# Performance work log

Hardware: AMD Instinct MI355X
Metric: run time of the kernel (lower is better)

The kernel has to match this reference:

```python
import jax, jax.numpy as jnp
import numpy as np

BEAMS, TEMP, DEPTH, K = 8, 0.4, 3, 3   # beams, router temperature, max_depth, n_experts
EPS, NEG = 1e-5, -1e9

def _conv(x, w, b):
    y = jax.lax.conv_general_dilated(x, w, (1, 1), 'VALID',
                                     dimension_numbers=('NCHW', 'OIHW', 'NCHW'))
    return y + b[None, :, None, None]

def _bn(x, g, b, m, v):
    inv = g * jax.lax.rsqrt(v + EPS)
    return x * inv[None, :, None, None] + (b - m * inv)[None, :, None, None]

def _pool(x):  # AvgPool2d(2)
    return jax.lax.reduce_window(x, 0.0, jax.lax.add, (1, 1, 2, 2), (1, 1, 2, 2), 'VALID') * 0.25

def _fwd(x, conv1_w, conv1_b, bn1_g, bn1_b, bn1_m, bn1_v,
         conv2_w, conv2_b, bn2_g, bn2_b, bn2_m, bn2_v,
         conv3_w, conv3_b, bn3_g, bn3_b, bn3_m, bn3_v,
         Wxh, Whh, bh, Who, bo, emb, Wexp, bexp, Wout, bout):
    B = x.shape[0]
    h = _pool(jax.nn.relu(_bn(_conv(x, conv1_w, conv1_b), bn1_g, bn1_b, bn1_m, bn1_v)))
    h = _pool(jax.nn.relu(_bn(_conv(h, conv2_w, conv2_b), bn2_g, bn2_b, bn2_m, bn2_v)))
    h = _pool(jax.nn.relu(_bn(_conv(h, conv3_w, conv3_b), bn3_g, bn3_b, bn3_m, bn3_v)))
    feat = h.reshape(B, -1)                                  # (B,128)
    # --- beam search over length-3 op sequences with RNN router ---
    hr = jnp.broadcast_to(feat[:, None, :], (B, BEAMS, 128))  # router hidden, (B,beams,128)
    scores = jnp.full((B, BEAMS), NEG, dtype=x.dtype).at[:, 0].set(0.0)
    ops_seq = []
    for _ in range(DEPTH):
        logits = jnp.einsum('bkd,do->bko', hr, Who) + bo      # (B,beams,3)
        logp = jax.nn.log_softmax(logits / TEMP, axis=-1)
        total = (scores[..., None] + logp).reshape(B, BEAMS * K)
        scores, idx = jax.lax.top_k(total, BEAMS)             # (B,beams)
        beam_idx, op = idx // K, idx % K
        hr = jnp.take_along_axis(hr, beam_idx[..., None], axis=1)
        hr = jnp.tanh(hr @ Whh + emb[op] @ Wxh + bh)
        ops_seq = [jnp.take_along_axis(o, beam_idx, axis=1) for o in ops_seq]
        ops_seq.append(op)
    # --- top-1 routed expert chain (grouped gather-GEMM instead of per-sample loop) ---
    hs = jnp.broadcast_to(feat[:, None, :], (B, BEAMS, 128)).reshape(B * BEAMS, 128)
    for op in ops_seq:
        o = op.reshape(B * BEAMS)
        hs = jax.nn.relu(jnp.einsum('nd,ndk->nk', hs, Wexp[o]) + bexp[o])
    return jax.nn.log_softmax(hs @ Wout + bout, axis=1)      # (B*beams,10)

def setup_inputs() -> dict:
    key = jax.random.key(0)
    ks = jax.random.split(key, 20)
    n = lambda i, shape, s: jax.random.normal(ks[i], shape, jnp.float32) * s
    d = {
        'x': jax.random.normal(ks[0], (512, 1, 32, 32), jnp.float32),
        'conv1_w': n(1, (32, 1, 3, 3), 0.2),  'conv1_b': n(2, (32,), 0.02),
        'bn1_g': jnp.ones((32,), jnp.float32), 'bn1_b': jnp.zeros((32,), jnp.float32),
        'bn1_m': jnp.zeros((32,), jnp.float32), 'bn1_v': jnp.ones((32,), jnp.float32),
        'conv2_w': n(3, (32, 32, 3, 3), 0.06), 'conv2_b': n(4, (32,), 0.02),
        'bn2_g': jnp.ones((32,), jnp.float32), 'bn2_b': jnp.zeros((32,), jnp.float32),
        'bn2_m': jnp.zeros((32,), jnp.float32), 'bn2_v': jnp.ones((32,), jnp.float32),
        'conv3_w': n(5, (32, 32, 3, 3), 0.06), 'conv3_b': n(6, (32,), 0.02),
        'bn3_g': jnp.ones((32,), jnp.float32), 'bn3_b': jnp.zeros((32,), jnp.float32),
        'bn3_m': jnp.zeros((32,), jnp.float32), 'bn3_v': jnp.ones((32,), jnp.float32),
        'Wxh': n(7, (128, 128), 0.09), 'Whh': n(8, (128, 128), 0.09), 'bh': n(9, (128,), 0.02),
        'Who': n(10, (128, 3), 0.09), 'bo': n(11, (3,), 0.02), 'emb': n(12, (3, 128), 0.5),
        'Wexp': n(13, (3, 128, 128), 0.09), 'bexp': n(14, (3, 128), 0.02),
        'Wout': n(15, (128, 10), 0.09), 'bout': n(16, (10,), 0.02),
    }
    return d

def reference(x, conv1_w, conv1_b, bn1_g, bn1_b, bn1_m, bn1_v,
              conv2_w, conv2_b, bn2_g, bn2_b, bn2_m, bn2_v,
              conv3_w, conv3_b, bn3_g, bn3_b, bn3_m, bn3_v,
              Wxh, Whh, bh, Who, bo, emb, Wexp, bexp, Wout, bout):
    return _fwd(x, conv1_w, conv1_b, bn1_g, bn1_b, bn1_m, bn1_v,
                conv2_w, conv2_b, bn2_g, bn2_b, bn2_m, bn2_v,
                conv3_w, conv3_b, bn3_g, bn3_b, bn3_m, bn3_v,
                Wxh, Whh, bh, Who, bo, emb, Wexp, bexp, Wout, bout)
```

## Files before the change

kernel.cpp:

```cpp
#include <hip/hip_runtime.h>
#include <math.h>

__global__ __launch_bounds__(512) void conv1_k(
    const float* __restrict__ x, const float* __restrict__ w,
    const float* __restrict__ cb, const float* __restrict__ bg,
    const float* __restrict__ bb, const float* __restrict__ bm,
    const float* __restrict__ bv, float* __restrict__ h1)
{
    __shared__ float img[32 * 33];
    __shared__ float ws_[288];
    __shared__ float scale[32], bias2[32];
    const int b = blockIdx.x, tid = threadIdx.x;
    for (int i = tid; i < 1024; i += 512) {
        const int y = i >> 5, xx = i & 31;
        img[y * 33 + xx] = x[b * 1024 + i];
    }
    if (tid < 288) ws_[tid] = w[tid];
    if (tid < 32) {
        float inv = bg[tid] / sqrtf(bv[tid] + 1e-5f);
        scale[tid] = inv;
        bias2[tid] = (cb[tid] - bm[tid]) * inv + bb[tid];
    }
    __syncthreads();

    const int co = tid >> 4, py = tid & 15;
    if (py < 15) {
        float acc0[30], acc1[30];
        #pragma unroll
        for (int i = 0; i < 30; ++i) { acc0[i] = 0.f; acc1[i] = 0.f; }
        const float* w9 = &ws_[co * 9];
        #pragma unroll
        for (int ir = 0; ir < 4; ++ir) {
            const int y = 2 * py + ir;
            float wk0 = 0.f, wk1 = 0.f, wk2 = 0.f, wl0 = 0.f, wl1 = 0.f, wl2 = 0.f;
            if (ir <= 2) { wk0 = w9[ir * 3 + 0]; wk1 = w9[ir * 3 + 1]; wk2 = w9[ir * 3 + 2]; }
            if (ir >= 1) { wl0 = w9[(ir - 1) * 3 + 0]; wl1 = w9[(ir - 1) * 3 + 1]; wl2 = w9[(ir - 1) * 3 + 2]; }
            #pragma unroll
            for (int xx = 0; xx < 32; ++xx) {
                const float rv = img[y * 33 + xx];
                if (ir <= 2) {
                    if (xx <= 29) acc0[xx] += rv * wk0;
                    if (xx >= 1 && xx <= 30) acc0[xx - 1] += rv * wk1;
                    if (xx >= 2) acc0[xx - 2] += rv * wk2;
                }
                if (ir >= 1) {
                    if (xx <= 29) acc1[xx] += rv * wl0;
                    if (xx >= 1 && xx <= 30) acc1[xx - 1] += rv * wl1;
                    if (xx >= 2) acc1[xx - 2] += rv * wl2;
                }
            }
        }
        const float sc = scale[co], bs = bias2[co];
        #pragma unroll
        for (int px = 0; px < 15; ++px) {
            const float v = fmaxf(acc0[2 * px] * sc + bs, 0.f)
                          + fmaxf(acc0[2 * px + 1] * sc + bs, 0.f)
                          + fmaxf(acc1[2 * px] * sc + bs, 0.f)
                          + fmaxf(acc1[2 * px + 1] * sc + bs, 0.f);
            h1[b * 7200 + co * 225 + py * 15 + px] = v * 0.25f;
        }
    }
}

__global__ __launch_bounds__(384) void conv2_k(
    const float* __restrict__ h1, const float* __restrict__ w,
    const float* __restrict__ cb, const float* __restrict__ bg,
    const float* __restrict__ bb, const float* __restrict__ bm,
    const float* __restrict__ bv, float* __restrict__ h2)
{
    __shared__ float in_s[32 * 210];
    __shared__ float w_s[9216];
    __shared__ float scale[32], bias2[32];
    const int b = blockIdx.x, tid = threadIdx.x;
    for (int i = tid; i < 6720; i += 384) {
        const int ci = i / 210, rem = i % 210;
        in_s[i] = h1[b * 7200 + ci * 225 + rem];
    }
    for (int i = tid; i < 9216; i += 384) {
        const int co = i & 31, k = i >> 5;
        w_s[i] = w[co * 288 + k];
    }
    if (tid < 32) {
        float inv = bg[tid] / sqrtf(bv[tid] + 1e-5f);
        scale[tid] = inv;
        bias2[tid] = (cb[tid] - bm[tid]) * inv + bb[tid];
    }
    __syncthreads();

    const int co = tid & 31, g = tid >> 5;
    const int py = g >> 1, xh = g & 1;
    const int gx0 = xh * 6;
    float acc0[6], acc1[6];
    #pragma unroll
    for (int i = 0; i < 6; ++i) { acc0[i] = 0.f; acc1[i] = 0.f; }

    for (int ci = 0; ci < 32; ++ci) {
        float w9[9];
        #pragma unroll
        for (int kk = 0; kk < 9; ++kk) w9[kk] = w_s[(ci * 9 + kk) * 32 + co];
        const float* ip = &in_s[ci * 210];
        #pragma unroll
        for (int ir = 0; ir < 4; ++ir) {
            const int y = 2 * py + ir;
            const float* rowp = &ip[y * 15 + gx0];
            #pragma unroll
            for (int xx = 0; xx < 8; ++xx) {
                const float rv = rowp[xx];
                if (ir <= 2) {
                    if (xx <= 5) acc0[xx] += rv * w9[ir * 3 + 0];
                    if (xx >= 1 && xx <= 6) acc0[xx - 1] += rv * w9[ir * 3 + 1];
                    if (xx >= 2) acc0[xx - 2] += rv * w9[ir * 3 + 2];
                }
                if (ir >= 1) {
                    if (xx <= 5) acc1[xx] += rv * w9[(ir - 1) * 3 + 0];
                    if (xx >= 1 && xx <= 6) acc1[xx - 1] += rv * w9[(ir - 1) * 3 + 1];
                    if (xx >= 2) acc1[xx - 2] += rv * w9[(ir - 1) * 3 + 2];
                }
            }
        }
    }
    const float sc = scale[co], bs = bias2[co];
    #pragma unroll
    for (int pxl = 0; pxl < 3; ++pxl) {
        const float v = fmaxf(acc0[2 * pxl] * sc + bs, 0.f)
                      + fmaxf(acc0[2 * pxl + 1] * sc + bs, 0.f)
                      + fmaxf(acc1[2 * pxl] * sc + bs, 0.f)
                      + fmaxf(acc1[2 * pxl + 1] * sc + bs, 0.f);
        h2[b * 1152 + co * 36 + py * 6 + xh * 3 + pxl] = v * 0.25f;
    }
}

__global__ __launch_bounds__(256) void conv3_k(
    const float* __restrict__ h2, const float* __restrict__ w,
    const float* __restrict__ cb, const float* __restrict__ bg,
    const float* __restrict__ bb, const float* __restrict__ bm,
    const float* __restrict__ bv, float* __restrict__ feat)
{
    __shared__ float in_s[1152];
    __shared__ float w_s[9216];
    __shared__ float psum[2][4][4][33];
    __shared__ float scale[32], bias2[32];
    const int b = blockIdx.x, tid = threadIdx.x;
    for (int i = tid; i < 1152; i += 256) in_s[i] = h2[b * 1152 + i];
    for (int i = tid; i < 9216; i += 256) {
        const int co = i & 31, k = i >> 5;
        w_s[i] = w[co * 288 + k];
    }
    if (tid < 32) {
        float inv = bg[tid] / sqrtf(bv[tid] + 1e-5f);
        scale[tid] = inv;
        bias2[tid] = (cb[tid] - bm[tid]) * inv + bb[tid];
    }
    __syncthreads();

    const int co = tid & 31, g = tid >> 5;
    const int pos = g & 3, h = g >> 2;
    const int y0 = (pos >> 1) * 2, x0 = (pos & 1) * 2;
    float s00 = 0.f, s01 = 0.f, s10 = 0.f, s11 = 0.f;
    for (int ci = h * 16; ci < h * 16 + 16; ++ci) {
        float w9[9];
        #pragma unroll
        for (int kk = 0; kk < 9; ++kk) w9[kk] = w_s[(ci * 9 + kk) * 32 + co];
        const float* ip = &in_s[ci * 36 + y0 * 6 + x0];
        float p[4][4];
        #pragma unroll
        for (int i = 0; i < 4; ++i)
            #pragma unroll
            for (int j = 0; j < 4; ++j)
                p[i][j] = ip[i * 6 + j];
        #pragma unroll
        for (int ky = 0; ky < 3; ++ky)
            #pragma unroll
            for (int kx = 0; kx < 3; ++kx) {
                const float wv = w9[ky * 3 + kx];
                s00 += p[ky][kx] * wv;
                s01 += p[ky][kx + 1] * wv;
                s10 += p[ky + 1][kx] * wv;
                s11 += p[ky + 1][kx + 1] * wv;
            }
    }
    psum[h][pos][0][co] = s00;
    psum[h][pos][1][co] = s01;
    psum[h][pos][2][co] = s10;
    psum[h][pos][3][co] = s11;
    __syncthreads();
    if (h == 0) {
        const float sc = scale[co], bs = bias2[co];
        float v = 0.f;
        #pragma unroll
        for (int k = 0; k < 4; ++k) {
            const float sk = psum[0][pos][k][co] + psum[1][pos][k][co];
            v += fmaxf(sk * sc + bs, 0.f);
        }
        feat[b * 128 + co * 4 + pos] = v * 0.25f;
    }
}

__global__ __launch_bounds__(384) void e2_k(
    const float* __restrict__ emb, const float* __restrict__ Wxh,
    const float* __restrict__ bh, float* __restrict__ E2)
{
    const int t = threadIdx.x;
    const int o = t >> 7, j = t & 127;
    float a = bh[j];
    float a2 = 0.f;
    #pragma unroll 4
    for (int d = 0; d < 64; ++d) {
        a  += emb[o * 128 + d] * Wxh[d * 128 + j];
        a2 += emb[o * 128 + d + 64] * Wxh[(d + 64) * 128 + j];
    }
    E2[t] = a + a2;
}

__global__ __launch_bounds__(512, 4) void router_k(
    const float* __restrict__ feat, const float* __restrict__ Whh,
    const float* __restrict__ Who, const float* __restrict__ bo,
    const float* __restrict__ E2, const float* __restrict__ Wexp,
    const float* __restrict__ bexp, const float* __restrict__ Wout,
    const float* __restrict__ bout, float* __restrict__ out)
{
    const int b = blockIdx.x, tid = threadIdx.x;
    const int j = tid & 127, q = tid >> 7;
    __shared__ float hbuf[2][8][128];
    __shared__ float E2s[3][128];
    __shared__ float bexps[3][128];
    __shared__ float psum[4][8][128];
    __shared__ float total[24], scores[8];
    __shared__ int bi[8], opsel[8], oph[3][8], oph2[3][8];

    const float fv = feat[b * 128 + j];
    hbuf[0][2 * q][j] = fv;
    hbuf[0][2 * q + 1][j] = fv;
    for (int i = tid; i < 384; i += 512) {
        (&E2s[0][0])[i] = E2[i];
        (&bexps[0][0])[i] = bexp[i];
    }
    if (tid < 8) scores[tid] = (tid == 0) ? 0.f : -1.0e9f;
    __syncthreads();

    int cur = 0;
    for (int t = 0; t < 3; ++t) {
        {
            const int grp = tid >> 5, l = tid & 31;
            if (grp < 8) {
                float p0 = 0.f, p1 = 0.f, p2 = 0.f;
                #pragma unroll
                for (int dd = 0; dd < 4; ++dd) {
                    const int d = l + 32 * dd;
                    const float hv = hbuf[cur][grp][d];
                    p0 += hv * Who[d * 3 + 0];
                    p1 += hv * Who[d * 3 + 1];
                    p2 += hv * Who[d * 3 + 2];
                }
                #pragma unroll
                for (int s = 16; s > 0; s >>= 1) {
                    p0 += __shfl_down(p0, s, 32);
                    p1 += __shfl_down(p1, s, 32);
                    p2 += __shfl_down(p2, s, 32);
                }
                if (l == 0) {
                    const float t0 = (p0 + bo[0]) / 0.4f;
                    const float t1 = (p1 + bo[1]) / 0.4f;
                    const float t2 = (p2 + bo[2]) / 0.4f;
                    const float mm = fmaxf(t0, fmaxf(t1, t2));
                    const float lse = mm + logf(expf(t0 - mm) + expf(t1 - mm) + expf(t2 - mm));
                    const float sc = scores[grp];
                    total[grp * 3 + 0] = sc + (t0 - lse);
                    total[grp * 3 + 1] = sc + (t1 - lse);
                    total[grp * 3 + 2] = sc + (t2 - lse);
                }
            }
        }
        __syncthreads();
        if (tid == 0) {
            float tv[24];
            #pragma unroll
            for (int i = 0; i < 24; ++i) tv[i] = total[i];
            unsigned mask = 0;
            for (int r = 0; r < 8; ++r) {
                float best = -INFINITY; int idx = 0;
                #pragma unroll
                for (int i = 0; i < 24; ++i) {
                    if (!(mask & (1u << i)) && tv[i] > best) { best = tv[i]; idx = i; }
                }
                mask |= 1u << idx;
                scores[r] = best;
                bi[r] = idx / 3;
                opsel[r] = idx % 3;
            }
            for (int r = 0; r < 8; ++r) {
                for (int s = 0; s < t; ++s) oph2[s][r] = oph[s][bi[r]];
                oph2[t][r] = opsel[r];
            }
            for (int r = 0; r < 8; ++r)
                for (int s = 0; s <= t; ++s) oph[s][r] = oph2[s][r];
        }
        __syncthreads();
        {
            const float* h0 = &hbuf[cur][bi[0]][0];
            const float* h1 = &hbuf[cur][bi[1]][0];
            const float* h2 = &hbuf[cur][bi[2]][0];
            const float* h3 = &hbuf[cur][bi[3]][0];
            const float* h4 = &hbuf[cur][bi[4]][0];
            const float* h5 = &hbuf[cur][bi[5]][0];
            const float* h6 = &hbuf[cur][bi[6]][0];
            const float* h7 = &hbuf[cur][bi[7]][0];
            float a0 = 0.f, a1 = 0.f, a2 = 0.f, a3 = 0.f, a4 = 0.f, a5 = 0.f, a6 = 0.f, a7 = 0.f;
            const int dbase = q * 32;
            const float* wp = &Whh[dbase * 128 + j];
            #pragma unroll 4
            for (int dd = 0; dd < 32; ++dd) {
                const int d = dbase + dd;
                const float wv = wp[dd * 128];
                a0 += h0[d] * wv; a1 += h1[d] * wv; a2 += h2[d] * wv; a3 += h3[d] * wv;
                a4 += h4[d] * wv; a5 += h5[d] * wv; a6 += h6[d] * wv; a7 += h7[d] * wv;
            }
            psum[q][0][j] = a0; psum[q][1][j] = a1; psum[q][2][j] = a2; psum[q][3][j] = a3;
            psum[q][4][j] = a4; psum[q][5][j] = a5; psum[q][6][j] = a6; psum[q][7][j] = a7;
        }
        __syncthreads();
        {
            const int nxt = cur ^ 1;
            #pragma unroll
            for (int rr = 0; rr < 2; ++rr) {
                const int r = 2 * q + rr;
                const float v = psum[0][r][j] + psum[1][r][j] + psum[2][r][j] + psum[3][r][j]
                              + E2s[opsel[r]][j];
                hbuf[nxt][r][j] = tanhf(v);
            }
        }
        cur ^= 1;
        __syncthreads();
    }

    hbuf[0][2 * q][j] = fv;
    hbuf[0][2 * q + 1][j] = fv;
    __syncthreads();
    int c2 = 0;
    for (int t = 0; t < 3; ++t) {
        const int o0 = oph[t][0], o1 = oph[t][1], o2 = oph[t][2], o3 = oph[t][3];
        const int o4 = oph[t][4], o5 = oph[t][5], o6 = oph[t][6], o7 = oph[t][7];
        {
            const float* h0 = &hbuf[c2][0][0];
            const float* h1 = &hbuf[c2][1][0];
            const float* h2 = &hbuf[c2][2][0];
            const float* h3 = &hbuf[c2][3][0];
            const float* h4 = &hbuf[c2][4][0];
            const float* h5 = &hbuf[c2][5][0];
            const float* h6 = &hbuf[c2][6][0];
            const float* h7 = &hbuf[c2][7][0];
            float a0 = 0.f, a1 = 0.f, a2 = 0.f, a3 = 0.f, a4 = 0.f, a5 = 0.f, a6 = 0.f, a7 = 0.f;
            const int dbase = q * 32;
            const float* wp = &Wexp[dbase * 128 + j];
            #pragma unroll 4
            for (int dd = 0; dd < 32; ++dd) {
                const int d = dbase + dd;
                const float w0 = wp[dd * 128];
                const float w1 = wp[dd * 128 + 16384];
                const float w2 = wp[dd * 128 + 32768];
                a0 += h0[d] * (o0 == 2 ? w2 : (o0 == 1 ? w1 : w0));
                a1 += h1[d] * (o1 == 2 ? w2 : (o1 == 1 ? w1 : w0));
                a2 += h2[d] * (o2 == 2 ? w2 : (o2 == 1 ? w1 : w0));
                a3 += h3[d] * (o3 == 2 ? w2 : (o3 == 1 ? w1 : w0));
                a4 += h4[d] * (o4 == 2 ? w2 : (o4 == 1 ? w1 : w0));
                a5 += h5[d] * (o5 == 2 ? w2 : (o5 == 1 ? w1 : w0));
                a6 += h6[d] * (o6 == 2 ? w2 : (o6 == 1 ? w1 : w0));
                a7 += h7[d] * (o7 == 2 ? w2 : (o7 == 1 ? w1 : w0));
            }
            psum[q][0][j] = a0; psum[q][1][j] = a1; psum[q][2][j] = a2; psum[q][3][j] = a3;
            psum[q][4][j] = a4; psum[q][5][j] = a5; psum[q][6][j] = a6; psum[q][7][j] = a7;
        }
        __syncthreads();
        {
            const int nxt = c2 ^ 1;
            #pragma unroll
            for (int rr = 0; rr < 2; ++rr) {
                const int r = 2 * q + rr;
                const float v = psum[0][r][j] + psum[1][r][j] + psum[2][r][j] + psum[3][r][j]
                              + bexps[oph[t][r]][j];
                hbuf[nxt][r][j] = fmaxf(v, 0.f);
            }
        }
        c2 ^= 1;
        __syncthreads();
    }

    {
        const int grp = tid >> 5, l = tid & 31;
        if (grp < 8) {
            float acc = 0.f;
            if (l < 10) {
                acc = bout[l];
                float acc2 = 0.f;
                const float* hrow = &hbuf[c2][grp][0];
                #pragma unroll 4
                for (int d = 0; d < 64; ++d) {
                    acc  += hrow[d] * Wout[d * 10 + l];
                    acc2 += hrow[d + 64] * Wout[(d + 64) * 10 + l];
                }
                acc += acc2;
            }
            float mm = (l < 10) ? acc : -INFINITY;
            #pragma unroll
            for (int s = 16; s > 0; s >>= 1) mm = fmaxf(mm, __shfl_xor(mm, s, 32));
            float ex = (l < 10) ? expf(acc - mm) : 0.f;
            float sum = ex;
            #pragma unroll
            for (int s = 16; s > 0; s >>= 1) sum += __shfl_xor(sum, s, 32);
            const float lse = mm + logf(sum);
            if (l < 10) out[(b * 8 + grp) * 10 + l] = acc - lse;
        }
    }
}

extern "C" void kernel_launch(void* const* d_in, const int* in_sizes, int n_in,
                              void* d_out, int out_size, void* d_ws, size_t ws_size,
                              hipStream_t stream) {
    (void)in_sizes; (void)n_in; (void)out_size; (void)ws_size;
    const float* x    = (const float*)d_in[0];
    const float* c1w  = (const float*)d_in[1];
    const float* c1b  = (const float*)d_in[2];
    const float* g1   = (const float*)d_in[3];
    const float* b1   = (const float*)d_in[4];
    const float* m1   = (const float*)d_in[5];
    const float* v1   = (const float*)d_in[6];
    const float* c2w  = (const float*)d_in[7];
    const float* c2b  = (const float*)d_in[8];
    const float* g2   = (const float*)d_in[9];
    const float* b2   = (const float*)d_in[10];
    const float* m2   = (const float*)d_in[11];
    const float* v2   = (const float*)d_in[12];
    const float* c3w  = (const float*)d_in[13];
    const float* c3b  = (const float*)d_in[14];
    const float* g3   = (const float*)d_in[15];
    const float* b3   = (const float*)d_in[16];
    const float* m3   = (const float*)d_in[17];
    const float* v3   = (const float*)d_in[18];
    const float* Wxh  = (const float*)d_in[19];
    const float* Whh  = (const float*)d_in[20];
    const float* bh   = (const float*)d_in[21];
    const float* Who  = (const float*)d_in[22];
    const float* bo   = (const float*)d_in[23];
    const float* emb  = (const float*)d_in[24];
    const float* Wexp = (const float*)d_in[25];
    const float* bexp = (const float*)d_in[26];
    const float* Wout = (const float*)d_in[27];
    const float* bout = (const float*)d_in[28];

    float* ws   = (float*)d_ws;
    float* h1   = ws;
    float* h2   = h1 + 3686400;
    float* feat = h2 + 589824;
    float* E2   = feat + 65536;

    e2_k<<<1, 384, 0, stream>>>(emb, Wxh, bh, E2);
    conv1_k<<<512, 512, 0, stream>>>(x, c1w, c1b, g1, b1, m1, v1, h1);
    conv2_k<<<512, 384, 0, stream>>>(h1, c2w, c2b, g2, b2, m2, v2, h2);
    conv3_k<<<512, 256, 0, stream>>>(h2, c3w, c3b, g3, b3, m3, v3, feat);
    router_k<<<512, 512, 0, stream>>>(feat, Whh, Who, bo, E2,
                                      Wexp, bexp, Wout, bout, (float*)d_out);
}
```

Baseline: 244.9 us.

## Pre-transpose conv weights once, restructure conv2 tiling, use readlane broadcasts in router

```diff
diff --git a/kernel.cpp b/kernel.cpp
--- a/kernel.cpp
+++ b/kernel.cpp
@@ -1,5 +1,38 @@
 #include <hip/hip_runtime.h>
 #include <math.h>
+
+__device__ __forceinline__ float rdlane(float v, int l) {
+    return __int_as_float(__builtin_amdgcn_readlane(__float_as_int(v), l));
+}
+
+__global__ __launch_bounds__(384) void wprep_k(
+    const float* __restrict__ c2w, const float* __restrict__ c3w,
+    const float* __restrict__ emb, const float* __restrict__ Wxh,
+    const float* __restrict__ bh,
+    float* __restrict__ w2t, float* __restrict__ w3t, float* __restrict__ E2)
+{
+    const int t = threadIdx.x, blk = blockIdx.x;
+    if (blk == 0) {
+        for (int i = t; i < 9216; i += 384) {
+            const int co = i & 31, k = i >> 5;
+            w2t[i] = c2w[co * 288 + k];
+        }
+    } else if (blk == 1) {
+        for (int i = t; i < 9216; i += 384) {
+            const int co = i & 31, k = i >> 5;
+            w3t[i] = c3w[co * 288 + k];
+        }
+    } else {
+        const int o = t >> 7, j = t & 127;
+        float a = bh[j], a2 = 0.f;
+        #pragma unroll 4
+        for (int d = 0; d < 64; ++d) {
+            a  += emb[o * 128 + d] * Wxh[d * 128 + j];
+            a2 += emb[o * 128 + d + 64] * Wxh[(d + 64) * 128 + j];
+        }
+        E2[t] = a + a2;
+    }
+}
 
 __global__ __launch_bounds__(512) void conv1_k(
     const float* __restrict__ x, const float* __restrict__ w,
@@ -62,94 +95,82 @@
     }
 }
 
-__global__ __launch_bounds__(384) void conv2_k(
-    const float* __restrict__ h1, const float* __restrict__ w,
+__global__ __launch_bounds__(192) void conv2_k(
+    const float* __restrict__ h1, const float* __restrict__ w2t,
     const float* __restrict__ cb, const float* __restrict__ bg,
     const float* __restrict__ bb, const float* __restrict__ bm,
     const float* __restrict__ bv, float* __restrict__ h2)
 {
-    __shared__ float in_s[32 * 210];
-    __shared__ float w_s[9216];
-    __shared__ float scale[32], bias2[32];
+    __shared__ float in_s[32 * 14 * 16];
     const int b = blockIdx.x, tid = threadIdx.x;
-    for (int i = tid; i < 6720; i += 384) {
+    for (int i = tid; i < 6720; i += 192) {
         const int ci = i / 210, rem = i % 210;
-        in_s[i] = h1[b * 7200 + ci * 225 + rem];
-    }
-    for (int i = tid; i < 9216; i += 384) {
-        const int co = i & 31, k = i >> 5;
-        w_s[i] = w[co * 288 + k];
-    }
-    if (tid < 32) {
-        float inv = bg[tid] / sqrtf(bv[tid] + 1e-5f);
-        scale[tid] = inv;
-        bias2[tid] = (cb[tid] - bm[tid]) * inv + bb[tid];
-    }
-    __syncthreads();
-
-    const int co = tid & 31, g = tid >> 5;
-    const int py = g >> 1, xh = g & 1;
-    const int gx0 = xh * 6;
-    float acc0[6], acc1[6];
+        const int row = rem / 15, col = rem % 15;
+        in_s[ci * 224 + row * 16 + col] = h1[b * 7200 + ci * 225 + rem];
+    }
+    __syncthreads();
+
+    const int co = tid & 31, py = tid >> 5;
+    float acc0[12], acc1[12];
     #pragma unroll
-    for (int i = 0; i < 6; ++i) { acc0[i] = 0.f; acc1[i] = 0.f; }
+    for (int i = 0; i < 12; ++i) { acc0[i] = 0.f; acc1[i] = 0.f; }
 
     for (int ci = 0; ci < 32; ++ci) {
         float w9[9];
-        #pragma unroll
-        for (int kk = 0; kk < 9; ++kk) w9[kk] = w_s[(ci * 9 + kk) * 32 + co];
-        const float* ip = &in_s[ci * 210];
+        const float* wk = &w2t[(ci * 9) * 32 + co];
+        #pragma unroll
+        for (int kk = 0; kk < 9; ++kk) w9[kk] = wk[kk * 32];
         #pragma unroll
         for (int ir = 0; ir < 4; ++ir) {
-            const int y = 2 * py + ir;
-            const float* rowp = &ip[y * 15 + gx0];
-            #pragma unroll
-            for (int xx = 0; xx < 8; ++xx) {
-                const float rv = rowp[xx];
-                if (ir <= 2) {
-                    if (xx <= 5) acc0[xx] += rv * w9[ir * 3 + 0];
-                    if (xx >= 1 && xx <= 6) acc0[xx - 1] += rv * w9[ir * 3 + 1];
-                    if (xx >= 2) acc0[xx - 2] += rv * w9[ir * 3 + 2];
-                }
-                if (ir >= 1) {
-                    if (xx <= 5) acc1[xx] += rv * w9[(ir - 1) * 3 + 0];
-                    if (xx >= 1 && xx <= 6) acc1[xx - 1] += rv * w9[(ir - 1) * 3 + 1];
-                    if (xx >= 2) acc1[xx - 2] += rv * w9[(ir - 1) * 3 + 2];
-                }
-            }
-        }
-    }
-    const float sc = scale[co], bs = bias2[co];
+            const float* rp = &in_s[ci * 224 + (2 * py + ir) * 16];
+            const float4 q0 = *reinterpret_cast<const float4*>(rp);
+            const float4 q1 = *reinterpret_cast<const float4*>(rp + 4);
+            const float4 q2 = *reinterpret_cast<const float4*>(rp + 8);
+            const float4 q3 = *reinterpret_cast<const float4*>(rp + 12);
+            float p[16];
+            p[0]=q0.x; p[1]=q0.y; p[2]=q0.z; p[3]=q0.w;
+            p[4]=q1.x; p[5]=q1.y; p[6]=q1.z; p[7]=q1.w;
+            p[8]=q2.x; p[9]=q2.y; p[10]=q2.z; p[11]=q2.w;
+            p[12]=q3.x; p[13]=q3.y; p[14]=q3.z; p[15]=q3.w;
+            if (ir <= 2) {
+                const float wa0 = w9[ir * 3], wa1 = w9[ir * 3 + 1], wa2 = w9[ir * 3 + 2];
+                #pragma unroll
+                for (int c = 0; c < 12; ++c)
+                    acc0[c] += p[c] * wa0 + p[c + 1] * wa1 + p[c + 2] * wa2;
+            }
+            if (ir >= 1) {
+                const float wb0 = w9[(ir - 1) * 3], wb1 = w9[(ir - 1) * 3 + 1], wb2 = w9[(ir - 1) * 3 + 2];
+                #pragma unroll
+                for (int c = 0; c < 12; ++c)
+                    acc1[c] += p[c] * wb0 + p[c + 1] * wb1 + p[c + 2] * wb2;
+            }
+        }
+    }
+    const float inv = bg[co] / sqrtf(bv[co] + 1e-5f);
+    const float bs = (cb[co] - bm[co]) * inv + bb[co];
     #pragma unroll
-    for (int pxl = 0; pxl < 3; ++pxl) {
-        const float v = fmaxf(acc0[2 * pxl] * sc + bs, 0.f)
-                      + fmaxf(acc0[2 * pxl + 1] * sc + bs, 0.f)
-                      + fmaxf(acc1[2 * pxl] * sc + bs, 0.f)
-                      + fmaxf(acc1[2 * pxl + 1] * sc + bs, 0.f);
-        h2[b * 1152 + co * 36 + py * 6 + xh * 3 + pxl] = v * 0.25f;
+    for (int px = 0; px < 6; ++px) {
+        const float v = fmaxf(acc0[2 * px] * inv + bs, 0.f)
+                      + fmaxf(acc0[2 * px + 1] * inv + bs, 0.f)
+                      + fmaxf(acc1[2 * px] * inv + bs, 0.f)
+                      + fmaxf(acc1[2 * px + 1] * inv + bs, 0.f);
+        h2[b * 1152 + co * 36 + py * 6 + px] = v * 0.25f;
     }
 }
 
 __global__ __launch_bounds__(256) void conv3_k(
-    const float* __restrict__ h2, const float* __restrict__ w,
+    const float* __restrict__ h2, const float* __restrict__ w3t,
     const float* __restrict__ cb, const float* __restrict__ bg,
     const float* __restrict__ bb, const float* __restrict__ bm,
     const float* __restrict__ bv, float* __restrict__ feat)
 {
-    __shared__ float in_s[1152];
-    __shared__ float w_s[9216];
+    __shared__ float in_s[32 * 48];
     __shared__ float psum[2][4][4][33];
-    __shared__ float scale[32], bias2[32];
     const int b = blockIdx.x, tid = threadIdx.x;
-    for (int i = tid; i < 1152; i += 256) in_s[i] = h2[b * 1152 + i];
-    for (int i = tid; i < 9216; i += 256) {
-        const int co = i & 31, k = i >> 5;
-        w_s[i] = w[co * 288 + k];
-    }
-    if (tid < 32) {
-        float inv = bg[tid] / sqrtf(bv[tid] + 1e-5f);
-        scale[tid] = inv;
-        bias2[tid] = (cb[tid] - bm[tid]) * inv + bb[tid];
+    for (int i = tid; i < 1152; i += 256) {
+        const int ci = i / 36, rem = i % 36;
+        const int row = rem / 6, col = rem % 6;
+        in_s[ci * 48 + row * 8 + col] = h2[b * 1152 + i];
     }
     __syncthreads();
 
@@ -159,15 +180,17 @@
     float s00 = 0.f, s01 = 0.f, s10 = 0.f, s11 = 0.f;
     for (int ci = h * 16; ci < h * 16 + 16; ++ci) {
         float w9[9];
-        #pragma unroll
-        for (int kk = 0; kk < 9; ++kk) w9[kk] = w_s[(ci * 9 + kk) * 32 + co];
-        const float* ip = &in_s[ci * 36 + y0 * 6 + x0];
+        const float* wk = &w3t[(ci * 9) * 32 + co];
+        #pragma unroll
+        for (int kk = 0; kk < 9; ++kk) w9[kk] = wk[kk * 32];
+        const int base = ci * 48 + y0 * 8 + x0;
         float p[4][4];
         #pragma unroll
-        for (int i = 0; i < 4; ++i)
-            #pragma unroll
-            for (int j = 0; j < 4; ++j)
-                p[i][j] = ip[i * 6 + j];
+        for (int i = 0; i < 4; ++i) {
+            const float2 a = *reinterpret_cast<const float2*>(&in_s[base + i * 8]);
+            const float2 c = *reinterpret_cast<const float2*>(&in_s[base + i * 8 + 2]);
+            p[i][0] = a.x; p[i][1] = a.y; p[i][2] = c.x; p[i][3] = c.y;
+        }
         #pragma unroll
         for (int ky = 0; ky < 3; ++ky)
             #pragma unroll
@@ -185,31 +208,16 @@
     psum[h][pos][3][co] = s11;
     __syncthreads();
     if (h == 0) {
-        const float sc = scale[co], bs = bias2[co];
+        const float inv = bg[co] / sqrtf(bv[co] + 1e-5f);
+        const float bs = (cb[co] - bm[co]) * inv + bb[co];
         float v = 0.f;
         #pragma unroll
         for (int k = 0; k < 4; ++k) {
             const float sk = psum[0][pos][k][co] + psum[1][pos][k][co];
-            v += fmaxf(sk * sc + bs, 0.f);
+            v += fmaxf(sk * inv + bs, 0.f);
         }
         feat[b * 128 + co * 4 + pos] = v * 0.25f;
     }
-}
-
-__global__ __launch_bounds__(384) void e2_k(
-    const float* __restrict__ emb, const float* __restrict__ Wxh,
-    const float* __restrict__ bh, float* __restrict__ E2)
-{
-    const int t = threadIdx.x;
-    const int o = t >> 7, j = t & 127;
-    float a = bh[j];
-    float a2 = 0.f;
-    #pragma unroll 4
-    for (int d = 0; d < 64; ++d) {
-        a  += emb[o * 128 + d] * Wxh[d * 128 + j];
-        a2 += emb[o * 128 + d + 64] * Wxh[(d + 64) * 128 + j];
-    }
-    E2[t] = a + a2;
 }
 
 __global__ __launch_bounds__(512, 4) void router_k(
@@ -220,7 +228,7 @@
     const float* __restrict__ bout, float* __restrict__ out)
 {
     const int b = blockIdx.x, tid = threadIdx.x;
-    const int j = tid & 127, q = tid >> 7;
+    const int j = tid & 127, q = tid >> 7, lane31 = tid & 31;
     __shared__ float hbuf[2][8][128];
     __shared__ float E2s[3][128];
     __shared__ float bexps[3][128];
@@ -238,6 +246,7 @@
     if (tid < 8) scores[tid] = (tid == 0) ? 0.f : -1.0e9f;
     __syncthreads();
 
+    const int dbase = q * 32;
     int cur = 0;
     for (int t = 0; t < 3; ++t) {
         {
@@ -297,23 +306,23 @@
         }
         __syncthreads();
         {
-            const float* h0 = &hbuf[cur][bi[0]][0];
-            const float* h1 = &hbuf[cur][bi[1]][0];
-            const float* h2 = &hbuf[cur][bi[2]][0];
-            const float* h3 = &hbuf[cur][bi[3]][0];
-            const float* h4 = &hbuf[cur][bi[4]][0];
-            const float* h5 = &hbuf[cur][bi[5]][0];
-            const float* h6 = &hbuf[cur][bi[6]][0];
-            const float* h7 = &hbuf[cur][bi[7]][0];
+            const float h0r = hbuf[cur][bi[0]][dbase + lane31];
+            const float h1r = hbuf[cur][bi[1]][dbase + lane31];
+            const float h2r = hbuf[cur][bi[2]][dbase + lane31];
+            const float h3r = hbuf[cur][bi[3]][dbase + lane31];
+            const float h4r = hbuf[cur][bi[4]][dbase + lane31];
+            const float h5r = hbuf[cur][bi[5]][dbase + lane31];
+            const float h6r = hbuf[cur][bi[6]][dbase + lane31];
+            const float h7r = hbuf[cur][bi[7]][dbase + lane31];
             float a0 = 0.f, a1 = 0.f, a2 = 0.f, a3 = 0.f, a4 = 0.f, a5 = 0.f, a6 = 0.f, a7 = 0.f;
-            const int dbase = q * 32;
             const float* wp = &Whh[dbase * 128 + j];
-            #pragma unroll 4
+            #pragma unroll
             for (int dd = 0; dd < 32; ++dd) {
-                const int d = dbase + dd;
                 const float wv = wp[dd * 128];
-                a0 += h0[d] * wv; a1 += h1[d] * wv; a2 += h2[d] * wv; a3 += h3[d] * wv;
-                a4 += h4[d] * wv; a5 += h5[d] * wv; a6 += h6[d] * wv; a7 += h7[d] * wv;
+                a0 += rdlane(h0r, dd) * wv; a1 += rdlane(h1r, dd) * wv;
+                a2 += rdlane(h2r, dd) * wv; a3 += rdlane(h3r, dd) * wv;
+                a4 += rdlane(h4r, dd) * wv; a5 += rdlane(h5r, dd) * wv;
+                a6 += rdlane(h6r, dd) * wv; a7 += rdlane(h7r, dd) * wv;
             }
             psum[q][0][j] = a0; psum[q][1][j] = a1; psum[q][2][j] = a2; psum[q][3][j] = a3;
             psum[q][4][j] = a4; psum[q][5][j] = a5; psum[q][6][j] = a6; psum[q][7][j] = a7;
@@ -338,34 +347,34 @@
     __syncthreads();
     int c2 = 0;
     for (int t = 0; t < 3; ++t) {
-        const int o0 = oph[t][0], o1 = oph[t][1], o2 = oph[t][2], o3 = oph[t][3];
-        const int o4 = oph[t][4], o5 = oph[t][5], o6 = oph[t][6], o7 = oph[t][7];
         {
-            const float* h0 = &hbuf[c2][0][0];
-            const float* h1 = &hbuf[c2][1][0];
-            const float* h2 = &hbuf[c2][2][0];
-            const float* h3 = &hbuf[c2][3][0];
-            const float* h4 = &hbuf[c2][4][0];
-            const float* h5 = &hbuf[c2][5][0];
-            const float* h6 = &hbuf[c2][6][0];
-            const float* h7 = &hbuf[c2][7][0];
+            const float h0r = hbuf[c2][0][dbase + lane31];
+            const float h1r = hbuf[c2][1][dbase + lane31];
+            const float h2r = hbuf[c2][2][dbase + lane31];
+            const float h3r = hbuf[c2][3][dbase + lane31];
+            const float h4r = hbuf[c2][4][dbase + lane31];
+            const float h5r = hbuf[c2][5][dbase + lane31];
+            const float h6r = hbuf[c2][6][dbase + lane31];
+            const float h7r = hbuf[c2][7][dbase + lane31];
+            const float* wp0 = &Wexp[oph[t][0] * 16384 + dbase * 128 + j];
+            const float* wp1 = &Wexp[oph[t][1] * 16384 + dbase * 128 + j];
+            const float* wp2 = &Wexp[oph[t][2] * 16384 + dbase * 128 + j];
+            const float* wp3 = &Wexp[oph[t][3] * 16384 + dbase * 128 + j];
+            const float* wp4 = &Wexp[oph[t][4] * 16384 + dbase * 128 + j];
+            const float* wp5 = &Wexp[oph[t][5] * 16384 + dbase * 128 + j];
+            const float* wp6 = &Wexp[oph[t][6] * 16384 + dbase * 128 + j];
+            const float* wp7 = &Wexp[oph[t][7] * 16384 + dbase * 128 + j];
             float a0 = 0.f, a1 = 0.f, a2 = 0.f, a3 = 0.f, a4 = 0.f, a5 = 0.f, a6 = 0.f, a7 = 0.f;
-            const int dbase = q * 32;
-            const float* wp = &Wexp[dbase * 128 + j];
-            #pragma unroll 4
+            #pragma unroll
             for (int dd = 0; dd < 32; ++dd) {
-                const int d = dbase + dd;
-                const float w0 = wp[dd * 128];
-                const float w1 = wp[dd * 128 + 16384];
-                const float w2 = wp[dd * 128 + 32768];
-                a0 += h0[d] * (o0 == 2 ? w2 : (o0 == 1 ? w1 : w0));
-                a1 += h1[d] * (o1 == 2 ? w2 : (o1 == 1 ? w1 : w0));
-                a2 += h2[d] * (o2 == 2 ? w2 : (o2 == 1 ? w1 : w0));
-                a3 += h3[d] * (o3 == 2 ? w2 : (o3 == 1 ? w1 : w0));
-                a4 += h4[d] * (o4 == 2 ? w2 : (o4 == 1 ? w1 : w0));
-                a5 += h5[d] * (o5 == 2 ? w2 : (o5 == 1 ? w1 : w0));
-                a6 += h6[d] * (o6 == 2 ? w2 : (o6 == 1 ? w1 : w0));
-                a7 += h7[d] * (o7 == 2 ? w2 : (o7 == 1 ? w1 : w0));
+                a0 += rdlane(h0r, dd) * wp0[dd * 128];
+                a1 += rdlane(h1r, dd) * wp1[dd * 128];
+                a2 += rdlane(h2r, dd) * wp2[dd * 128];
+                a3 += rdlane(h3r, dd) * wp3[dd * 128];
+                a4 += rdlane(h4r, dd) * wp4[dd * 128];
+                a5 += rdlane(h5r, dd) * wp5[dd * 128];
+                a6 += rdlane(h6r, dd) * wp6[dd * 128];
+                a7 += rdlane(h7r, dd) * wp7[dd * 128];
             }
             psum[q][0][j] = a0; psum[q][1][j] = a1; psum[q][2][j] = a2; psum[q][3][j] = a3;
             psum[q][4][j] = a4; psum[q][5][j] = a5; psum[q][6][j] = a6; psum[q][7][j] = a7;
@@ -452,11 +461,13 @@
     float* h2   = h1 + 3686400;
     float* feat = h2 + 589824;
     float* E2   = feat + 65536;
-
-    e2_k<<<1, 384, 0, stream>>>(emb, Wxh, bh, E2);
+    float* w2t  = E2 + 384;
+    float* w3t  = w2t + 9216;
+
+    wprep_k<<<3, 384, 0, stream>>>(c2w, c3w, emb, Wxh, bh, w2t, w3t, E2);
     conv1_k<<<512, 512, 0, stream>>>(x, c1w, c1b, g1, b1, m1, v1, h1);
-    conv2_k<<<512, 384, 0, stream>>>(h1, c2w, c2b, g2, b2, m2, v2, h2);
-    conv3_k<<<512, 256, 0, stream>>>(h2, c3w, c3b, g3, b3, m3, v3, feat);
+    conv2_k<<<512, 192, 0, stream>>>(h1, w2t, c2b, g2, b2, m2, v2, h2);
+    conv3_k<<<512, 256, 0, stream>>>(h2, w3t, c3b, g3, b3, m3, v3, feat);
     router_k<<<512, 512, 0, stream>>>(feat, Whh, Who, bo, E2,
                                       Wexp, bexp, Wout, bout, (float*)d_out);
 }
```

Result: slower. 285.4 us (+16.6%).
